# Optimization experiments

Hardware: AMD Instinct MI355X
Metric: run time of the kernel (lower is better)

The kernel has to match this reference:

```python
import jax, jax.numpy as jnp
import numpy as np

N_NODES = 2048
IN_FEATURES = 1024
N_HEADS = 8
N_HIDDEN = 32  # out_features // n_heads = 256 // 8
NEG_SLOPE = 0.2


def setup_inputs() -> dict:
    key = jax.random.key(0)
    k1, k2, k3, k4 = jax.random.split(key, 4)
    h = jax.random.normal(k1, (N_NODES, IN_FEATURES), dtype=jnp.float32)
    adj_mat = jax.random.randint(k2, (N_NODES, N_NODES, 1), 0, 2).astype(jnp.int32)
    W = jax.random.normal(k3, (IN_FEATURES, N_HEADS * N_HIDDEN), dtype=jnp.float32) * (1.0 / np.sqrt(IN_FEATURES))
    a = jax.random.normal(k4, (2 * N_HIDDEN,), dtype=jnp.float32) * (1.0 / np.sqrt(2 * N_HIDDEN))
    return {"h": h, "adj_mat": adj_mat, "W": W, "a": a}


def reference(h, adj_mat, W, a):
    n = h.shape[0]
    # g: [n, heads, hidden]
    g = (h @ W).reshape(n, N_HEADS, N_HIDDEN)
    # attn Linear on concat([g_i, g_j]) is linear => split weight: e_ij = a_l.g_i + a_r.g_j
    a_l, a_r = a[:N_HIDDEN], a[N_HIDDEN:]
    s_l = jnp.einsum('ihf,f->ih', g, a_l)  # [n, heads]
    s_r = jnp.einsum('jhf,f->jh', g, a_r)  # [n, heads]
    e = s_l[:, None, :] + s_r[None, :, :]  # [n, n, heads]
    e = jnp.where(e >= 0, e, NEG_SLOPE * e)  # leaky relu
    e = jnp.where(adj_mat == 0, -jnp.inf, e)
    att = jax.nn.softmax(e, axis=1)  # softmax over source nodes j
    out = jnp.einsum('ijh,jhf->ihf', att, g)  # [n, heads, hidden]
    return out.reshape(n, N_HEADS * N_HIDDEN)
```

## Files before the change

kernel.cpp:

```cpp
#include <hip/hip_runtime.h>
#include <hip/hip_bf16.h>
#include <math.h>

#define N_NODES 2048
#define IN_F    1024
#define NH      8
#define HF      32
#define OUTF    256
#define LOG2E   1.4426950408889634f

typedef __attribute__((ext_vector_type(8))) short short8;
typedef __attribute__((ext_vector_type(4))) short short4v;
typedef __attribute__((ext_vector_type(4))) float f32x4;

__device__ __forceinline__ short f2bf(float x) {
  unsigned u = __float_as_uint(x);
  return (short)((u + 0x7FFFu + ((u >> 16) & 1u)) >> 16);
}
__device__ __forceinline__ float bf2f(short b) {
  return __uint_as_float(((unsigned)(unsigned short)b) << 16);
}
__device__ __forceinline__ float fexp2(float x) {
#if __has_builtin(__builtin_amdgcn_exp2f)
  return __builtin_amdgcn_exp2f(x);
#else
  return exp2f(x);
#endif
}

__global__ __launch_bounds__(256)
void prep_kernel(const float* __restrict__ h, const int* __restrict__ adj,
                 const float* __restrict__ W, short* __restrict__ h_hi,
                 short* __restrict__ wt_hi, short* __restrict__ wt_lo,
                 unsigned* __restrict__ bits) {
  const int T = blockIdx.x * 256 + threadIdx.x;
  {
    const float4 v0 = *(const float4*)(h + T * 8);
    const float4 v1 = *(const float4*)(h + T * 8 + 4);
    const float x[8] = {v0.x, v0.y, v0.z, v0.w, v1.x, v1.y, v1.z, v1.w};
    short8 hi;
    #pragma unroll
    for (int j = 0; j < 8; ++j) hi[j] = f2bf(x[j]);
    *(short8*)(h_hi + T * 8) = hi;
  }
  if (T < (OUTF * IN_F / 8)) {
    const int kgrp = T >> 8, n = T & 255;
    #pragma unroll
    for (int j = 0; j < 8; ++j) {
      const float x = W[(kgrp * 8 + j) * OUTF + n];
      const short hb = f2bf(x);
      wt_hi[n * IN_F + kgrp * 8 + j] = hb;
      wt_lo[n * IN_F + kgrp * 8 + j] = f2bf(x - bf2f(hb));
    }
  }
  if (T < (N_NODES * 64)) {
    const int4* p = (const int4*)(adj + (T >> 6) * N_NODES + (T & 63) * 32);
    unsigned wbits = 0;
    #pragma unroll
    for (int v = 0; v < 8; ++v) {
      const int4 x = p[v];
      wbits |= (x.x != 0 ? 1u : 0u) << (4 * v + 0);
      wbits |= (x.y != 0 ? 1u : 0u) << (4 * v + 1);
      wbits |= (x.z != 0 ? 1u : 0u) << (4 * v + 2);
      wbits |= (x.w != 0 ? 1u : 0u) << (4 * v + 3);
    }
    bits[T] = wbits;
  }
}

__global__ __launch_bounds__(512)
void gemm_scores_kernel(const short* __restrict__ h_hi,
                        const short* __restrict__ wt_hi, const short* __restrict__ wt_lo,
                        const float* __restrict__ a, short* __restrict__ gt,
                        float* __restrict__ s_l, float* __restrict__ s_r_t) {
  __shared__ float xbuf[4][64][8];
  const int bid = blockIdx.x;
  const int mb = bid >> 2;
  const int nb = bid & 3;
  const int w = threadIdx.x >> 6;
  const int l = threadIdx.x & 63;
  const int il = l & 15, q = l >> 4;
  const int wm = w >> 2;
  const int hp = (w >> 1) & 1;
  const int ks = w & 1;
  const int hh = nb * 2 + hp;
  const int rowb = mb * 32 + wm * 16;
  const int kb = ks * (IN_F / 2);

  const short* ah  = h_hi + (rowb + il) * IN_F + kb;
  const short* bh0 = wt_hi + (hh * HF + il) * IN_F + kb;
  const short* bl0 = wt_lo + (hh * HF + il) * IN_F + kb;
  const short* bh1 = bh0 + 16 * IN_F;
  const short* bl1 = bl0 + 16 * IN_F;

  f32x4 acc0 = {0.f, 0.f, 0.f, 0.f};
  f32x4 acc1 = {0.f, 0.f, 0.f, 0.f};
  #pragma unroll 4
  for (int k0 = 0; k0 < IN_F / 2; k0 += 32) {
    const short8 a_h  = *(const short8*)(ah + k0 + 8 * q);
    const short8 b_h0 = *(const short8*)(bh0 + k0 + 8 * q);
    const short8 b_l0 = *(const short8*)(bl0 + k0 + 8 * q);
    const short8 b_h1 = *(const short8*)(bh1 + k0 + 8 * q);
    const short8 b_l1 = *(const short8*)(bl1 + k0 + 8 * q);
    acc0 = __builtin_amdgcn_mfma_f32_16x16x32_bf16(a_h, b_h0, acc0, 0, 0, 0);
    acc0 = __builtin_amdgcn_mfma_f32_16x16x32_bf16(a_h, b_l0, acc0, 0, 0, 0);
    acc1 = __builtin_amdgcn_mfma_f32_16x16x32_bf16(a_h, b_h1, acc1, 0, 0, 0);
    acc1 = __builtin_amdgcn_mfma_f32_16x16x32_bf16(a_h, b_l1, acc1, 0, 0, 0);
  }

  const int t = w >> 1;
  if (ks == 1) {
    *(f32x4*)&xbuf[t][l][0] = acc0;
    *(f32x4*)&xbuf[t][l][4] = acc1;
  }
  __syncthreads();
  if (ks == 1) return;
  {
    const f32x4 u0 = *(const f32x4*)&xbuf[t][l][0];
    const f32x4 u1 = *(const f32x4*)&xbuf[t][l][4];
    #pragma unroll
    for (int r = 0; r < 4; ++r) { acc0[r] += u0[r]; acc1[r] += u1[r]; }
  }

  {
    short4v p0, p1;
    #pragma unroll
    for (int r = 0; r < 4; ++r) { p0[r] = f2bf(acc0[r]); p1[r] = f2bf(acc1[r]); }
    *(short4v*)(gt + (hh * HF + il) * N_NODES + rowb + 4 * q)      = p0;
    *(short4v*)(gt + (hh * HF + 16 + il) * N_NODES + rowb + 4 * q) = p1;
  }

  const float alv0 = a[il], alv1 = a[16 + il];
  const float arv0 = a[HF + il], arv1 = a[HF + 16 + il];
  float sl[4], sr[4];
  #pragma unroll
  for (int r = 0; r < 4; ++r) {
    sl[r] = acc0[r] * alv0 + acc1[r] * alv1;
    sr[r] = acc0[r] * arv0 + acc1[r] * arv1;
  }
  #pragma unroll
  for (int off = 8; off >= 1; off >>= 1) {
    #pragma unroll
    for (int r = 0; r < 4; ++r) {
      sl[r] += __shfl_xor(sl[r], off, 64);
      sr[r] += __shfl_xor(sr[r], off, 64);
    }
  }
  if (il == 0) {
    #pragma unroll
    for (int r = 0; r < 4; ++r) {
      const int node = rowb + 4 * q + r;
      s_l[node * NH + hh] = sl[r] * LOG2E;
      s_r_t[hh * N_NODES + node] = sr[r] * LOG2E;
    }
  }
}

__global__ __launch_bounds__(512)
void attn_mfma_kernel(const unsigned* __restrict__ bits, const short* __restrict__ gt,
                      const float* __restrict__ s_l, const float* __restrict__ s_r_t,
                      float* __restrict__ out) {
  __shared__ float accbuf[7][64][16];
  __shared__ float dbuf[7][64][2];
  const int i0 = (blockIdx.x >> 3) * 32;
  const int hh = blockIdx.x & 7;
  const int js = threadIdx.x >> 6;
  const int l  = threadIdx.x & 63;
  const int il = l & 15;
  const int q  = l >> 4;

  const float slv0 = s_l[(i0 + il) * NH + hh];
  const float slv1 = s_l[(i0 + 16 + il) * NH + hh];
  const unsigned* bitrow0 = bits + (i0 + il) * 64;
  const unsigned* bitrow1 = bits + (i0 + 16 + il) * 64;
  const float* srh = s_r_t + hh * N_NODES;
  const short* g0p = gt + (hh * HF + il) * N_NODES;
  const short* g1p = gt + (hh * HF + 16 + il) * N_NODES;

  f32x4 acc00 = {0.f,0.f,0.f,0.f};
  f32x4 acc01 = {0.f,0.f,0.f,0.f};
  f32x4 acc10 = {0.f,0.f,0.f,0.f};
  f32x4 acc11 = {0.f,0.f,0.f,0.f};
  float d0 = 0.f, d1 = 0.f;

  const int jbase = js * (N_NODES / 8);
  #pragma unroll 2
  for (int j0 = jbase; j0 < jbase + N_NODES / 8; j0 += 32) {
    const unsigned wq0 = bitrow0[j0 >> 5] >> (8 * q);
    const unsigned wq1 = bitrow1[j0 >> 5] >> (8 * q);
    const float4 sra = *(const float4*)(srh + j0 + 8 * q);
    const float4 srb = *(const float4*)(srh + j0 + 8 * q + 4);
    const float sr_[8] = {sra.x, sra.y, sra.z, sra.w, srb.x, srb.y, srb.z, srb.w};
    short8 af0, af1;
    #pragma unroll
    for (int r = 0; r < 8; ++r) {
      float e0 = slv0 + sr_[r];
      e0 = fmaxf(e0, 0.2f * e0);
      const float w0 = ((wq0 >> r) & 1u) ? fexp2(e0) : 0.f;
      const short wb0 = f2bf(w0);
      af0[r] = wb0;
      d0 += bf2f(wb0);
      float e1 = slv1 + sr_[r];
      e1 = fmaxf(e1, 0.2f * e1);
      const float w1 = ((wq1 >> r) & 1u) ? fexp2(e1) : 0.f;
      const short wb1 = f2bf(w1);
      af1[r] = wb1;
      d1 += bf2f(wb1);
    }
    const short8 b0 = *(const short8*)(g0p + j0 + 8 * q);
    const short8 b1 = *(const short8*)(g1p + j0 + 8 * q);
    acc00 = __builtin_amdgcn_mfma_f32_16x16x32_bf16(af0, b0, acc00, 0, 0, 0);
    acc01 = __builtin_amdgcn_mfma_f32_16x16x32_bf16(af0, b1, acc01, 0, 0, 0);
    acc10 = __builtin_amdgcn_mfma_f32_16x16x32_bf16(af1, b0, acc10, 0, 0, 0);
    acc11 = __builtin_amdgcn_mfma_f32_16x16x32_bf16(af1, b1, acc11, 0, 0, 0);
  }

  d0 += __shfl_xor(d0, 16, 64);
  d0 += __shfl_xor(d0, 32, 64);
  d1 += __shfl_xor(d1, 16, 64);
  d1 += __shfl_xor(d1, 32, 64);

  if (js) {
    float* ab = &accbuf[js - 1][l][0];
    *(f32x4*)(ab + 0)  = acc00;
    *(f32x4*)(ab + 4)  = acc01;
    *(f32x4*)(ab + 8)  = acc10;
    *(f32x4*)(ab + 12) = acc11;
    dbuf[js - 1][l][0] = d0;
    dbuf[js - 1][l][1] = d1;
  }
  __syncthreads();
  if (js) return;

  float t0 = d0, t1 = d1;
  #pragma unroll
  for (int s = 0; s < 7; ++s) {
    const float* ab = &accbuf[s][l][0];
    const f32x4 u00 = *(const f32x4*)(ab + 0);
    const f32x4 u01 = *(const f32x4*)(ab + 4);
    const f32x4 u10 = *(const f32x4*)(ab + 8);
    const f32x4 u11 = *(const f32x4*)(ab + 12);
    #pragma unroll
    for (int r = 0; r < 4; ++r) {
      acc00[r] += u00[r]; acc01[r] += u01[r];
      acc10[r] += u10[r]; acc11[r] += u11[r];
    }
    t0 += dbuf[s][l][0];
    t1 += dbuf[s][l][1];
  }
  #pragma unroll
  for (int r = 0; r < 4; ++r) {
    const int row0 = i0 + 4 * q + r;
    const int row1 = i0 + 16 + 4 * q + r;
    const float inv0 = 1.0f / __shfl(t0, 4 * q + r, 64);
    const float inv1 = 1.0f / __shfl(t1, 4 * q + r, 64);
    out[row0 * OUTF + hh * HF + il]      = acc00[r] * inv0;
    out[row0 * OUTF + hh * HF + 16 + il] = acc01[r] * inv0;
    out[row1 * OUTF + hh * HF + il]      = acc10[r] * inv1;
    out[row1 * OUTF + hh * HF + 16 + il] = acc11[r] * inv1;
  }
}

extern "C" void kernel_launch(void* const* d_in, const int* in_sizes, int n_in,
                              void* d_out, int out_size, void* d_ws, size_t ws_size,
                              hipStream_t stream) {
  const float* h   = (const float*)d_in[0];
  const int*   adj = (const int*)d_in[1];
  const float* W   = (const float*)d_in[2];
  const float* a   = (const float*)d_in[3];
  float* out = (float*)d_out;

  float* s_l   = (float*)d_ws;
  float* s_r_t = s_l + N_NODES * NH;
  unsigned* bits = (unsigned*)(s_r_t + NH * N_NODES);
  short* gt    = (short*)(bits + N_NODES * 64);
  short* h_hi  = gt + NH * HF * N_NODES;
  short* wt_hi = h_hi + N_NODES * IN_F;
  short* wt_lo = wt_hi + OUTF * IN_F;

  prep_kernel<<<1024, 256, 0, stream>>>(h, adj, W, h_hi, wt_hi, wt_lo, bits);
  gemm_scores_kernel<<<256, 512, 0, stream>>>(h_hi, wt_hi, wt_lo, a, gt, s_l, s_r_t);
  attn_mfma_kernel<<<512, 512, 0, stream>>>(bits, gt, s_l, s_r_t, out);
}
```

Baseline: 50.24 us.

## Fuse h bf16 conversion into GEMM and retile attention to 64 rows per block

The separate pass that converts h to bf16 in the prep kernel is removed; the GEMM now loads fp32 h directly and rounds to bf16 in registers, which avoids writing and re-reading a 4 MB intermediate. The prep grid is halved to match the remaining adjacency and weight work. The attention kernel now handles 64 destination rows per block in two row groups of 4 warps, each warp covering a quarter of the source nodes instead of an eighth. This halves the block count and shrinks the cross-warp reduction, and each warp keeps a longer serial loop.

```diff
diff --git a/kernel.cpp b/kernel.cpp
--- a/kernel.cpp
+++ b/kernel.cpp
@@ -29,20 +29,10 @@
 }
 
 __global__ __launch_bounds__(256)
-void prep_kernel(const float* __restrict__ h, const int* __restrict__ adj,
-                 const float* __restrict__ W, short* __restrict__ h_hi,
+void prep_kernel(const int* __restrict__ adj, const float* __restrict__ W,
                  short* __restrict__ wt_hi, short* __restrict__ wt_lo,
                  unsigned* __restrict__ bits) {
   const int T = blockIdx.x * 256 + threadIdx.x;
-  {
-    const float4 v0 = *(const float4*)(h + T * 8);
-    const float4 v1 = *(const float4*)(h + T * 8 + 4);
-    const float x[8] = {v0.x, v0.y, v0.z, v0.w, v1.x, v1.y, v1.z, v1.w};
-    short8 hi;
-    #pragma unroll
-    for (int j = 0; j < 8; ++j) hi[j] = f2bf(x[j]);
-    *(short8*)(h_hi + T * 8) = hi;
-  }
   if (T < (OUTF * IN_F / 8)) {
     const int kgrp = T >> 8, n = T & 255;
     #pragma unroll
@@ -53,7 +43,7 @@
       wt_lo[n * IN_F + kgrp * 8 + j] = f2bf(x - bf2f(hb));
     }
   }
-  if (T < (N_NODES * 64)) {
+  {
     const int4* p = (const int4*)(adj + (T >> 6) * N_NODES + (T & 63) * 32);
     unsigned wbits = 0;
     #pragma unroll
@@ -69,7 +59,7 @@
 }
 
 __global__ __launch_bounds__(512)
-void gemm_scores_kernel(const short* __restrict__ h_hi,
+void gemm_scores_kernel(const float* __restrict__ h,
                         const short* __restrict__ wt_hi, const short* __restrict__ wt_lo,
                         const float* __restrict__ a, short* __restrict__ gt,
                         float* __restrict__ s_l, float* __restrict__ s_r_t) {
@@ -87,7 +77,7 @@
   const int rowb = mb * 32 + wm * 16;
   const int kb = ks * (IN_F / 2);
 
-  const short* ah  = h_hi + (rowb + il) * IN_F + kb;
+  const float* ahf = h + (rowb + il) * IN_F + kb;
   const short* bh0 = wt_hi + (hh * HF + il) * IN_F + kb;
   const short* bl0 = wt_lo + (hh * HF + il) * IN_F + kb;
   const short* bh1 = bh0 + 16 * IN_F;
@@ -97,7 +87,13 @@
   f32x4 acc1 = {0.f, 0.f, 0.f, 0.f};
   #pragma unroll 4
   for (int k0 = 0; k0 < IN_F / 2; k0 += 32) {
-    const short8 a_h  = *(const short8*)(ah + k0 + 8 * q);
+    const float4 av0 = *(const float4*)(ahf + k0 + 8 * q);
+    const float4 av1 = *(const float4*)(ahf + k0 + 8 * q + 4);
+    short8 a_h;
+    a_h[0] = f2bf(av0.x); a_h[1] = f2bf(av0.y);
+    a_h[2] = f2bf(av0.z); a_h[3] = f2bf(av0.w);
+    a_h[4] = f2bf(av1.x); a_h[5] = f2bf(av1.y);
+    a_h[6] = f2bf(av1.z); a_h[7] = f2bf(av1.w);
     const short8 b_h0 = *(const short8*)(bh0 + k0 + 8 * q);
     const short8 b_l0 = *(const short8*)(bl0 + k0 + 8 * q);
     const short8 b_h1 = *(const short8*)(bh1 + k0 + 8 * q);
@@ -160,19 +156,22 @@
 void attn_mfma_kernel(const unsigned* __restrict__ bits, const short* __restrict__ gt,
                       const float* __restrict__ s_l, const float* __restrict__ s_r_t,
                       float* __restrict__ out) {
-  __shared__ float accbuf[7][64][16];
-  __shared__ float dbuf[7][64][2];
-  const int i0 = (blockIdx.x >> 3) * 32;
+  __shared__ float accbuf[2][3][64][16];
+  __shared__ float dbuf[2][3][64][2];
+  const int i0 = (blockIdx.x >> 3) * 64;
   const int hh = blockIdx.x & 7;
-  const int js = threadIdx.x >> 6;
+  const int w  = threadIdx.x >> 6;
+  const int ig = w >> 2;
+  const int js = w & 3;
   const int l  = threadIdx.x & 63;
   const int il = l & 15;
   const int q  = l >> 4;
-
-  const float slv0 = s_l[(i0 + il) * NH + hh];
-  const float slv1 = s_l[(i0 + 16 + il) * NH + hh];
-  const unsigned* bitrow0 = bits + (i0 + il) * 64;
-  const unsigned* bitrow1 = bits + (i0 + 16 + il) * 64;
+  const int ib = i0 + ig * 32;
+
+  const float slv0 = s_l[(ib + il) * NH + hh];
+  const float slv1 = s_l[(ib + 16 + il) * NH + hh];
+  const unsigned* bitrow0 = bits + (ib + il) * 64;
+  const unsigned* bitrow1 = bits + (ib + 16 + il) * 64;
   const float* srh = s_r_t + hh * N_NODES;
   const short* g0p = gt + (hh * HF + il) * N_NODES;
   const short* g1p = gt + (hh * HF + 16 + il) * N_NODES;
@@ -183,9 +182,9 @@
   f32x4 acc11 = {0.f,0.f,0.f,0.f};
   float d0 = 0.f, d1 = 0.f;
 
-  const int jbase = js * (N_NODES / 8);
+  const int jbase = js * (N_NODES / 4);
   #pragma unroll 2
-  for (int j0 = jbase; j0 < jbase + N_NODES / 8; j0 += 32) {
+  for (int j0 = jbase; j0 < jbase + N_NODES / 4; j0 += 32) {
     const unsigned wq0 = bitrow0[j0 >> 5] >> (8 * q);
     const unsigned wq1 = bitrow1[j0 >> 5] >> (8 * q);
     const float4 sra = *(const float4*)(srh + j0 + 8 * q);
@@ -221,21 +220,21 @@
   d1 += __shfl_xor(d1, 32, 64);
 
   if (js) {
-    float* ab = &accbuf[js - 1][l][0];
+    float* ab = &accbuf[ig][js - 1][l][0];
     *(f32x4*)(ab + 0)  = acc00;
     *(f32x4*)(ab + 4)  = acc01;
     *(f32x4*)(ab + 8)  = acc10;
     *(f32x4*)(ab + 12) = acc11;
-    dbuf[js - 1][l][0] = d0;
-    dbuf[js - 1][l][1] = d1;
+    dbuf[ig][js - 1][l][0] = d0;
+    dbuf[ig][js - 1][l][1] = d1;
   }
   __syncthreads();
   if (js) return;
 
   float t0 = d0, t1 = d1;
   #pragma unroll
-  for (int s = 0; s < 7; ++s) {
-    const float* ab = &accbuf[s][l][0];
+  for (int s = 0; s < 3; ++s) {
+    const float* ab = &accbuf[ig][s][l][0];
     const f32x4 u00 = *(const f32x4*)(ab + 0);
     const f32x4 u01 = *(const f32x4*)(ab + 4);
     const f32x4 u10 = *(const f32x4*)(ab + 8);
@@ -245,13 +244,13 @@
       acc00[r] += u00[r]; acc01[r] += u01[r];
       acc10[r] += u10[r]; acc11[r] += u11[r];
     }
-    t0 += dbuf[s][l][0];
-    t1 += dbuf[s][l][1];
+    t0 += dbuf[ig][s][l][0];
+    t1 += dbuf[ig][s][l][1];
   }
   #pragma unroll
   for (int r = 0; r < 4; ++r) {
-    const int row0 = i0 + 4 * q + r;
-    const int row1 = i0 + 16 + 4 * q + r;
+    const int row0 = ib + 4 * q + r;
+    const int row1 = ib + 16 + 4 * q + r;
     const float inv0 = 1.0f / __shfl(t0, 4 * q + r, 64);
     const float inv1 = 1.0f / __shfl(t1, 4 * q + r, 64);
     out[row0 * OUTF + hh * HF + il]      = acc00[r] * inv0;
@@ -274,11 +273,10 @@
   float* s_r_t = s_l + N_NODES * NH;
   unsigned* bits = (unsigned*)(s_r_t + NH * N_NODES);
   short* gt    = (short*)(bits + N_NODES * 64);
-  short* h_hi  = gt + NH * HF * N_NODES;
-  short* wt_hi = h_hi + N_NODES * IN_F;
+  short* wt_hi = gt + NH * HF * N_NODES;
   short* wt_lo = wt_hi + OUTF * IN_F;
 
-  prep_kernel<<<1024, 256, 0, stream>>>(h, adj, W, h_hi, wt_hi, wt_lo, bits);
-  gemm_scores_kernel<<<256, 512, 0, stream>>>(h_hi, wt_hi, wt_lo, a, gt, s_l, s_r_t);
-  attn_mfma_kernel<<<512, 512, 0, stream>>>(bits, gt, s_l, s_r_t, out);
-}
+  prep_kernel<<<512, 256, 0, stream>>>(adj, W, wt_hi, wt_lo, bits);
+  gemm_scores_kernel<<<256, 512, 0, stream>>>(h, wt_hi, wt_lo, a, gt, s_l, s_r_t);
+  attn_mfma_kernel<<<256, 512, 0, stream>>>(bits, gt, s_l, s_r_t, out);
+}
```

Measured after the change: 53.02 us. 5.5% more time.
